# Kernel tuning notes

Measured on AMD Instinct MI355X. Metric: run time of the kernel, lower is better.

The kernel has to match this reference:

```python
import jax, jax.numpy as jnp
import numpy as np

BATCH, E = 4096, 8
DIMS = [512, 1024, 1024, 512]


def setup_inputs() -> dict:
    key = jax.random.key(0)
    ks = jax.random.split(key, 8)
    inp = {
        'weight_blend': jax.random.uniform(ks[0], (BATCH, E), dtype=jnp.float32),
        'x': jax.random.normal(ks[1], (BATCH, DIMS[0]), dtype=jnp.float32),
    }
    for i in range(3):
        inp[f'W{i}'] = jax.random.normal(ks[2 + i], (E, DIMS[i + 1], DIMS[i]), dtype=jnp.float32)
        inp[f'B{i}'] = jnp.zeros((E, DIMS[i + 1]), dtype=jnp.float32)
    return inp


def _blended_layer(weight_blend, x, W, B):
    # Fused form of: weight = sum_e blend[b,e]*W[e]; y = bmm(weight, x) + sum_e blend[b,e]*B[e]
    # Computed as sum_e blend_e * (W_e @ x) without materializing (batch,out,in).
    y = jnp.einsum('eoi,bi->beo', W, x)          # per-expert GEMM, (B,E,out)
    y = jnp.einsum('be,beo->bo', weight_blend, y)  # blend combine
    return y + weight_blend @ B                   # blended bias (B,out)


def reference(weight_blend, x, W0, B0, W1, B1, W2, B2):
    # Dropout with keep_prob=0.0 is identity in eval mode; activations: elu, elu, linear.
    h = jax.nn.elu(_blended_layer(weight_blend, x, W0, B0))
    h = jax.nn.elu(_blended_layer(weight_blend, h, W1, B1))
    out = _blended_layer(weight_blend, h, W2, B2)
    return out
```

## Files before the change

kernel.cpp:

```cpp
#include <hip/hip_runtime.h>
#include <cstdint>
#include <cstddef>

typedef __bf16 bf16x8 __attribute__((ext_vector_type(8)));
typedef float f32x4 __attribute__((ext_vector_type(4)));
typedef unsigned short u16;
typedef unsigned short u16x8 __attribute__((ext_vector_type(8)));

#define BATCH 4096
#define NE 8

__device__ __forceinline__ u16 f2bf(float f) {
  union { float f; uint32_t u; } v; v.f = f;
  uint32_t u = v.u;
  u += 0x7fffu + ((u >> 16) & 1u);
  return (u16)(u >> 16);
}

__device__ __forceinline__ float bf2f(u16 u) {
  union { uint32_t u; float f; } v; v.u = ((uint32_t)u) << 16;
  return v.f;
}

__device__ __forceinline__ void cast8(const float* src, u16* dst) {
  const float4* p = (const float4*)src;
  float4 a = p[0], b = p[1];
  u16x8 o;
  o[0] = f2bf(a.x); o[1] = f2bf(a.y); o[2] = f2bf(a.z); o[3] = f2bf(a.w);
  o[4] = f2bf(b.x); o[5] = f2bf(b.y); o[6] = f2bf(b.z); o[7] = f2bf(b.w);
  *(u16x8*)dst = o;
}

__device__ __forceinline__ void conv_w_chunk(const float* __restrict__ W,
                                             u16* __restrict__ Bt,
                                             int N, int K0, int chunk) {
  int per_row = K0 >> 3;
  int rid = chunk / per_row;
  int i0 = (chunk - rid * per_row) << 3;
  int e = rid / N;
  int o = rid - e * N;
  cast8(W + (size_t)rid * K0 + i0,
        Bt + (size_t)o * ((size_t)NE * K0) + (size_t)e * K0 + i0);
}

__global__ void prep_kernel(const float* __restrict__ x,
                            const float* __restrict__ W0,
                            const float* __restrict__ W1,
                            const float* __restrict__ W2,
                            u16* __restrict__ h0, u16* __restrict__ Bt0,
                            u16* __restrict__ Bt1, u16* __restrict__ Bt2) {
  int t = blockIdx.x * blockDim.x + threadIdx.x;
  const int C0 = BATCH * 512 / 8;
  const int C1 = C0 + NE * 1024 * 512 / 8;
  const int C2 = C1 + NE * 1024 * 1024 / 8;
  if (t < C0) {
    cast8(x + (size_t)t * 8, h0 + (size_t)t * 8);
  } else if (t < C1) {
    conv_w_chunk(W0, Bt0, 1024, 512, t - C0);
  } else if (t < C2) {
    conv_w_chunk(W1, Bt1, 1024, 1024, t - C1);
  } else {
    conv_w_chunk(W2, Bt2, 512, 1024, t - C2);
  }
}

template<int SLICES, bool ELU_ACT, bool OUT_BF16>
__global__ void combineS_kernel(const u16* __restrict__ P,
                                const float* __restrict__ blend,
                                const float* __restrict__ Bias,
                                void* __restrict__ outp, int N) {
  int t = blockIdx.x * blockDim.x + threadIdx.x;
  int per_row = N >> 3;
  int b = t / per_row;
  int i0 = (t - b * per_row) << 3;
  const size_t slice = (size_t)BATCH * N;
  float v[8] = {0, 0, 0, 0, 0, 0, 0, 0};
  #pragma unroll
  for (int s = 0; s < SLICES; ++s) {
    u16x8 pv = *(const u16x8*)(P + (size_t)s * slice + (size_t)b * N + i0);
    #pragma unroll
    for (int j = 0; j < 8; ++j) v[j] += bf2f(pv[j]);
  }
  const float4* blp = (const float4*)(blend + b * NE);
  float4 u0 = blp[0], u1 = blp[1];
  float bl[8] = {u0.x, u0.y, u0.z, u0.w, u1.x, u1.y, u1.z, u1.w};
  #pragma unroll
  for (int e = 0; e < NE; ++e) {
    const float4* bp = (const float4*)(Bias + (size_t)e * N + i0);
    float4 ba = bp[0], bb = bp[1];
    float bv[8] = {ba.x, ba.y, ba.z, ba.w, bb.x, bb.y, bb.z, bb.w};
    #pragma unroll
    for (int j = 0; j < 8; ++j) v[j] += bl[e] * bv[j];
  }
  if (ELU_ACT) {
    #pragma unroll
    for (int j = 0; j < 8; ++j) v[j] = v[j] > 0.f ? v[j] : expm1f(v[j]);
  }
  if (OUT_BF16) {
    u16x8 o;
    #pragma unroll
    for (int j = 0; j < 8; ++j) o[j] = f2bf(v[j]);
    *(u16x8*)((u16*)outp + (size_t)b * N + i0) = o;
  } else {
    float4* op = (float4*)((float*)outp + (size_t)b * N + i0);
    op[0] = (float4){v[0], v[1], v[2], v[3]};
    op[1] = (float4){v[4], v[5], v[6], v[7]};
  }
}

#define GL2LDS(g, l) __builtin_amdgcn_global_load_lds( \
    (__attribute__((address_space(1))) void*)(g),      \
    (__attribute__((address_space(3))) void*)(l), 16, 0, 0)

template<int K0, int EPB>
__global__ __launch_bounds__(256, 2)
void gemm_fold_kernel(const u16* __restrict__ h, const u16* __restrict__ Bt,
                      const float* __restrict__ blend,
                      u16* __restrict__ P, int N) {
  __shared__ __align__(16) u16 Hs[128 * 64];
  __shared__ __align__(16) u16 Bs[128 * 64];
  __shared__ float bls[128 * 9];

  const int tid  = threadIdx.x;
  const int w    = tid >> 6, lane = tid & 63;
  const int wm   = w >> 1,   wn   = w & 1;
  const int lrow = lane & 15, quad = lane >> 4;

  const int row0 = blockIdx.x * 128;
  const int col0 = blockIdx.y * 128;
  const int e0   = blockIdx.z * EPB;
  const int EK   = K0 * NE;

  {
    const float4 bv = ((const float4*)(blend + (size_t)row0 * NE))[tid];
    int row = tid >> 1, c0 = (tid & 1) * 4;
    bls[row * 9 + c0 + 0] = bv.x;
    bls[row * 9 + c0 + 1] = bv.y;
    bls[row * 9 + c0 + 2] = bv.z;
    bls[row * 9 + c0 + 3] = bv.w;
  }

  const int trow = tid >> 3;
  const int tcol = (tid & 7) ^ (trow & 7);
  const u16* gH = h + (size_t)(row0 + trow) * K0 + (tcol << 3);
  const u16* gB = Bt + (size_t)(col0 + trow) * EK + (size_t)e0 * K0 + (tcol << 3);
  u16* lH = &Hs[tid * 8];
  u16* lB = &Bs[tid * 8];

  const int xr = lrow & 7;
  const u16* fH[2][4];
  const u16* fB[2][4];
  #pragma unroll
  for (int kc = 0; kc < 2; ++kc)
    #pragma unroll
    for (int i = 0; i < 4; ++i) {
      fH[kc][i] = &Hs[(wm * 64 + i * 16 + lrow) * 64 + (((kc * 4 + quad) ^ xr) << 3)];
      fB[kc][i] = &Bs[(wn * 64 + i * 16 + lrow) * 64 + (((kc * 4 + quad) ^ xr) << 3)];
    }

  f32x4 acc[4][4];
  #pragma unroll
  for (int i = 0; i < 4; ++i)
    #pragma unroll
    for (int j = 0; j < 4; ++j) acc[i][j] = (f32x4){0.f, 0.f, 0.f, 0.f};

  #pragma unroll 1
  for (int ee = 0; ee < EPB; ++ee) {
    f32x4 acc2[4][4];
    #pragma unroll
    for (int i = 0; i < 4; ++i)
      #pragma unroll
      for (int j = 0; j < 4; ++j) acc2[i][j] = (f32x4){0.f, 0.f, 0.f, 0.f};

    const u16* pH = gH;
    const u16* pB = gB + (size_t)ee * K0;

    for (int it = 0; it < K0 / 64; ++it) {
      #pragma unroll
      for (int i = 0; i < 4; ++i) {
        GL2LDS(pH + (size_t)(32 * i) * K0, lH + 2048 * i);
        GL2LDS(pB + (size_t)(32 * i) * EK, lB + 2048 * i);
      }
      pH += 64; pB += 64;
      __syncthreads();

      #pragma unroll
      for (int kc = 0; kc < 2; ++kc) {
        bf16x8 hf[4], bfr[4];
        #pragma unroll
        for (int i = 0; i < 4; ++i) hf[i] = *(const bf16x8*)fH[kc][i];
        #pragma unroll
        for (int j = 0; j < 4; ++j) bfr[j] = *(const bf16x8*)fB[kc][j];
        #pragma unroll
        for (int i = 0; i < 4; ++i)
          #pragma unroll
          for (int j = 0; j < 4; ++j)
            acc2[i][j] = __builtin_amdgcn_mfma_f32_16x16x32_bf16(hf[i], bfr[j], acc2[i][j], 0, 0, 0);
      }
      __syncthreads();
    }

    #pragma unroll
    for (int mt = 0; mt < 4; ++mt) {
      float bl[4];
      #pragma unroll
      for (int r = 0; r < 4; ++r)
        bl[r] = bls[(wm * 64 + mt * 16 + quad * 4 + r) * 9 + (e0 + ee)];
      #pragma unroll
      for (int nt = 0; nt < 4; ++nt)
        #pragma unroll
        for (int r = 0; r < 4; ++r)
          acc[mt][nt][r] += bl[r] * acc2[mt][nt][r];
    }
  }

  u16* Ps = P + (size_t)blockIdx.z * ((size_t)BATCH * N);
  u16* ls = &Hs[w * 2048];
  #pragma unroll
  for (int half = 0; half < 2; ++half) {
    #pragma unroll
    for (int mh = 0; mh < 2; ++mh) {
      int mt = half * 2 + mh;
      #pragma unroll
      for (int r = 0; r < 4; ++r) {
        int rloc = mh * 16 + quad * 4 + r;
        #pragma unroll
        for (int nt = 0; nt < 4; ++nt) {
          int col = nt * 16 + lrow;
          int c8 = (col >> 3) ^ (rloc & 7);
          ls[rloc * 64 + (c8 << 3) + (col & 7)] = f2bf(acc[mt][nt][r]);
        }
      }
    }
    #pragma unroll
    for (int p = 0; p < 4; ++p) {
      int rloc = p * 8 + (lane >> 3);
      int c8 = (lane & 7) ^ (rloc & 7);
      u16x8 v = *(const u16x8*)&ls[rloc * 64 + (c8 << 3)];
      int row = row0 + wm * 64 + half * 32 + rloc;
      int colg = col0 + wn * 64 + ((lane & 7) << 3);
      *(u16x8*)&Ps[(size_t)row * N + colg] = v;
    }
  }
}

extern "C" void kernel_launch(void* const* d_in, const int* in_sizes, int n_in,
                              void* d_out, int out_size, void* d_ws, size_t ws_size,
                              hipStream_t stream) {
  const float* blend = (const float*)d_in[0];
  const float* x  = (const float*)d_in[1];
  const float* W0 = (const float*)d_in[2];
  const float* B0 = (const float*)d_in[3];
  const float* W1 = (const float*)d_in[4];
  const float* B1 = (const float*)d_in[5];
  const float* W2 = (const float*)d_in[6];
  const float* B2 = (const float*)d_in[7];
  float* out = (float*)d_out;

  char* ws = (char*)d_ws;
  u16* hA  = (u16*)ws;
  u16* h1  = (u16*)(ws + 8388608);
  u16* Bt0 = (u16*)(ws + 16777216);
  u16* Bt1 = (u16*)(ws + 25165824);
  u16* Bt2 = (u16*)(ws + 41943040);
  u16* P   = (u16*)(ws + 50331648);

  prep_kernel<<<9216, 256, 0, stream>>>(x, W0, W1, W2, hA, Bt0, Bt1, Bt2);

  gemm_fold_kernel<512, 4><<<dim3(32, 8, 2), 256, 0, stream>>>(hA, Bt0, blend, P, 1024);
  combineS_kernel<2, true, true><<<2048, 256, 0, stream>>>(P, blend, B0, h1, 1024);

  gemm_fold_kernel<1024, 4><<<dim3(32, 8, 2), 256, 0, stream>>>(h1, Bt1, blend, P, 1024);
  combineS_kernel<2, true, true><<<2048, 256, 0, stream>>>(P, blend, B1, hA, 1024);

  gemm_fold_kernel<1024, 2><<<dim3(32, 4, 4), 256, 0, stream>>>(hA, Bt2, blend, P, 512);
  combineS_kernel<4, false, false><<<1024, 256, 0, stream>>>(P, blend, B2, out, 512);
}
```

Baseline: 287.5 us.

## Pre-swizzle operands into MFMA fragment layout and drop LDS staging in GEMM

Prep and combine kernels now write activations and weights in a 16x32 fragment-tiled layout, so each lane can load its MFMA operand directly from global memory. The GEMM no longer stages tiles through LDS and no longer needs barriers in the K loop. The per-expert blend is folded with a ratio rescaling (acc *= blend_e/blend_{e+1}) so a single accumulator set is kept instead of two. This removes the LDS round trip and the barriers, at the cost of the cache reuse that shared tiles provided. The ratio trick is numerically fragile: blend is clamped at 1e-30, and division by small weights can amplify error.

After: 293.8 us. 1.02x slower.

```diff
diff --git a/kernel.cpp b/kernel.cpp
--- a/kernel.cpp
+++ b/kernel.cpp
@@ -31,40 +31,44 @@
   *(u16x8*)dst = o;
 }
 
-__device__ __forceinline__ void conv_w_chunk(const float* __restrict__ W,
-                                             u16* __restrict__ Bt,
-                                             int N, int K0, int chunk) {
-  int per_row = K0 >> 3;
-  int rid = chunk / per_row;
-  int i0 = (chunk - rid * per_row) << 3;
-  int e = rid / N;
-  int o = rid - e * N;
-  cast8(W + (size_t)rid * K0 + i0,
-        Bt + (size_t)o * ((size_t)NE * K0) + (size_t)e * K0 + i0);
-}
 
 __global__ void prep_kernel(const float* __restrict__ x,
                             const float* __restrict__ W0,
                             const float* __restrict__ W1,
                             const float* __restrict__ W2,
-                            u16* __restrict__ h0, u16* __restrict__ Bt0,
+                            u16* __restrict__ h0f, u16* __restrict__ Bt0,
                             u16* __restrict__ Bt1, u16* __restrict__ Bt2) {
   int t = blockIdx.x * blockDim.x + threadIdx.x;
-  const int C0 = BATCH * 512 / 8;
-  const int C1 = C0 + NE * 1024 * 512 / 8;
-  const int C2 = C1 + NE * 1024 * 1024 / 8;
+  const int C0 = 262144;
+  const int C1 = C0 + 524288;
+  const int C2 = C1 + 1048576;
   if (t < C0) {
-    cast8(x + (size_t)t * 8, h0 + (size_t)t * 8);
+    int lane = t & 63, c = t >> 6;
+    int rowt = c >> 4, kb = c & 15;
+    const float* s = x + ((size_t)(rowt * 16 + (lane & 15)) * 512 + kb * 32 + ((lane >> 4) << 3));
+    cast8(s, h0f + (size_t)c * 512 + (lane << 3));
   } else if (t < C1) {
-    conv_w_chunk(W0, Bt0, 1024, 512, t - C0);
+    int u = t - C0, lane = u & 63, c = u >> 6;
+    int kb = c & 15, c2 = c >> 4;
+    int colt = c2 & 63, e = c2 >> 6;
+    const float* s = W0 + (((size_t)e * 1024 + colt * 16 + (lane & 15)) * 512 + kb * 32 + ((lane >> 4) << 3));
+    cast8(s, Bt0 + (size_t)c * 512 + (lane << 3));
   } else if (t < C2) {
-    conv_w_chunk(W1, Bt1, 1024, 1024, t - C1);
+    int u = t - C1, lane = u & 63, c = u >> 6;
+    int kb = c & 31, c2 = c >> 5;
+    int colt = c2 & 63, e = c2 >> 6;
+    const float* s = W1 + (((size_t)e * 1024 + colt * 16 + (lane & 15)) * 1024 + kb * 32 + ((lane >> 4) << 3));
+    cast8(s, Bt1 + (size_t)c * 512 + (lane << 3));
   } else {
-    conv_w_chunk(W2, Bt2, 512, 1024, t - C2);
-  }
-}
-
-template<int SLICES, bool ELU_ACT, bool OUT_BF16>
+    int u = t - C2, lane = u & 63, c = u >> 6;
+    int kb = c & 31, c2 = c >> 5;
+    int colt = c2 & 31, e = c2 >> 5;
+    const float* s = W2 + (((size_t)e * 512 + colt * 16 + (lane & 15)) * 1024 + kb * 32 + ((lane >> 4) << 3));
+    cast8(s, Bt2 + (size_t)c * 512 + (lane << 3));
+  }
+}
+
+template<int SLICES, bool ELU_ACT, int KN>
 __global__ void combineS_kernel(const u16* __restrict__ P,
                                 const float* __restrict__ blend,
                                 const float* __restrict__ Bias,
@@ -96,11 +100,13 @@
     #pragma unroll
     for (int j = 0; j < 8; ++j) v[j] = v[j] > 0.f ? v[j] : expm1f(v[j]);
   }
-  if (OUT_BF16) {
+  if (KN > 0) {
     u16x8 o;
     #pragma unroll
     for (int j = 0; j < 8; ++j) o[j] = f2bf(v[j]);
-    *(u16x8*)((u16*)outp + (size_t)b * N + i0) = o;
+    int rowt = b >> 4, kb = i0 >> 5;
+    int lane = (b & 15) + (((i0 >> 3) & 3) << 4);
+    *(u16x8*)((u16*)outp + ((size_t)(rowt * (KN >> 5) + kb)) * 512 + (lane << 3)) = o;
   } else {
     float4* op = (float4*)((float*)outp + (size_t)b * N + i0);
     op[0] = (float4){v[0], v[1], v[2], v[3]};
@@ -108,55 +114,38 @@
   }
 }
 
-#define GL2LDS(g, l) __builtin_amdgcn_global_load_lds( \
-    (__attribute__((address_space(1))) void*)(g),      \
-    (__attribute__((address_space(3))) void*)(l), 16, 0, 0)
-
 template<int K0, int EPB>
 __global__ __launch_bounds__(256, 2)
-void gemm_fold_kernel(const u16* __restrict__ h, const u16* __restrict__ Bt,
-                      const float* __restrict__ blend,
-                      u16* __restrict__ P, int N) {
-  __shared__ __align__(16) u16 Hs[128 * 64];
-  __shared__ __align__(16) u16 Bs[128 * 64];
-  __shared__ float bls[128 * 9];
+void gemm_ff_kernel(const u16* __restrict__ Af, const u16* __restrict__ Btf,
+                    const float* __restrict__ blend, u16* __restrict__ P, int N) {
+  constexpr int KB = K0 / 32;
+  __shared__ float rat[128 * EPB];
+  __shared__ __align__(16) u16 ls[4 * 2048];
 
   const int tid  = threadIdx.x;
   const int w    = tid >> 6, lane = tid & 63;
   const int wm   = w >> 1,   wn   = w & 1;
   const int lrow = lane & 15, quad = lane >> 4;
-
   const int row0 = blockIdx.x * 128;
   const int col0 = blockIdx.y * 128;
   const int e0   = blockIdx.z * EPB;
-  const int EK   = K0 * NE;
-
-  {
-    const float4 bv = ((const float4*)(blend + (size_t)row0 * NE))[tid];
-    int row = tid >> 1, c0 = (tid & 1) * 4;
-    bls[row * 9 + c0 + 0] = bv.x;
-    bls[row * 9 + c0 + 1] = bv.y;
-    bls[row * 9 + c0 + 2] = bv.z;
-    bls[row * 9 + c0 + 3] = bv.w;
-  }
-
-  const int trow = tid >> 3;
-  const int tcol = (tid & 7) ^ (trow & 7);
-  const u16* gH = h + (size_t)(row0 + trow) * K0 + (tcol << 3);
-  const u16* gB = Bt + (size_t)(col0 + trow) * EK + (size_t)e0 * K0 + (tcol << 3);
-  u16* lH = &Hs[tid * 8];
-  u16* lB = &Bs[tid * 8];
-
-  const int xr = lrow & 7;
-  const u16* fH[2][4];
-  const u16* fB[2][4];
-  #pragma unroll
-  for (int kc = 0; kc < 2; ++kc)
-    #pragma unroll
-    for (int i = 0; i < 4; ++i) {
-      fH[kc][i] = &Hs[(wm * 64 + i * 16 + lrow) * 64 + (((kc * 4 + quad) ^ xr) << 3)];
-      fB[kc][i] = &Bs[(wn * 64 + i * 16 + lrow) * 64 + (((kc * 4 + quad) ^ xr) << 3)];
-    }
+  const int NT   = N >> 4;
+
+  for (int t = tid; t < 128 * EPB; t += 256) {
+    int row = t / EPB, j = t % EPB;
+    float sa = fmaxf(blend[(size_t)(row0 + row) * NE + e0 + j], 1e-30f);
+    float sb = (j < EPB - 1) ? fmaxf(blend[(size_t)(row0 + row) * NE + e0 + j + 1], 1e-30f) : 1.0f;
+    rat[t] = sa / sb;
+  }
+  __syncthreads();
+
+  const u16* aA[4];
+  const u16* aB[4];
+  #pragma unroll
+  for (int i = 0; i < 4; ++i) {
+    aA[i] = Af  + ((size_t)(blockIdx.x * 8 + wm * 4 + i) * KB) * 512 + (lane << 3);
+    aB[i] = Btf + ((size_t)((e0 * NT) + blockIdx.y * 8 + wn * 4 + i) * KB) * 512 + (lane << 3);
+  }
 
   f32x4 acc[4][4];
   #pragma unroll
@@ -166,56 +155,45 @@
 
   #pragma unroll 1
   for (int ee = 0; ee < EPB; ++ee) {
-    f32x4 acc2[4][4];
-    #pragma unroll
-    for (int i = 0; i < 4; ++i)
-      #pragma unroll
-      for (int j = 0; j < 4; ++j) acc2[i][j] = (f32x4){0.f, 0.f, 0.f, 0.f};
-
-    const u16* pH = gH;
-    const u16* pB = gB + (size_t)ee * K0;
-
-    for (int it = 0; it < K0 / 64; ++it) {
-      #pragma unroll
-      for (int i = 0; i < 4; ++i) {
-        GL2LDS(pH + (size_t)(32 * i) * K0, lH + 2048 * i);
-        GL2LDS(pB + (size_t)(32 * i) * EK, lB + 2048 * i);
-      }
-      pH += 64; pB += 64;
-      __syncthreads();
-
-      #pragma unroll
-      for (int kc = 0; kc < 2; ++kc) {
-        bf16x8 hf[4], bfr[4];
-        #pragma unroll
-        for (int i = 0; i < 4; ++i) hf[i] = *(const bf16x8*)fH[kc][i];
-        #pragma unroll
-        for (int j = 0; j < 4; ++j) bfr[j] = *(const bf16x8*)fB[kc][j];
+    #pragma unroll 1
+    for (int kq = 0; kq < KB / 4; ++kq) {
+      #pragma unroll
+      for (int u = 0; u < 4; ++u) {
+        bf16x8 fa[4], fb[4];
+        #pragma unroll
+        for (int i = 0; i < 4; ++i) fa[i] = *(const bf16x8*)(aA[i] + u * 512);
+        #pragma unroll
+        for (int j = 0; j < 4; ++j) fb[j] = *(const bf16x8*)(aB[j] + u * 512);
         #pragma unroll
         for (int i = 0; i < 4; ++i)
           #pragma unroll
           for (int j = 0; j < 4; ++j)
-            acc2[i][j] = __builtin_amdgcn_mfma_f32_16x16x32_bf16(hf[i], bfr[j], acc2[i][j], 0, 0, 0);
+            acc[i][j] = __builtin_amdgcn_mfma_f32_16x16x32_bf16(fa[i], fb[j], acc[i][j], 0, 0, 0);
       }
-      __syncthreads();
-    }
-
+      #pragma unroll
+      for (int i = 0; i < 4; ++i) { aA[i] += 2048; aB[i] += 2048; }
+    }
     #pragma unroll
     for (int mt = 0; mt < 4; ++mt) {
-      float bl[4];
+      float rr[4];
       #pragma unroll
       for (int r = 0; r < 4; ++r)
-        bl[r] = bls[(wm * 64 + mt * 16 + quad * 4 + r) * 9 + (e0 + ee)];
+        rr[r] = rat[(wm * 64 + mt * 16 + quad * 4 + r) * EPB + ee];
       #pragma unroll
       for (int nt = 0; nt < 4; ++nt)
         #pragma unroll
         for (int r = 0; r < 4; ++r)
-          acc[mt][nt][r] += bl[r] * acc2[mt][nt][r];
+          acc[mt][nt][r] *= rr[r];
+    }
+    #pragma unroll
+    for (int i = 0; i < 4; ++i) {
+      aA[i] -= (size_t)KB * 512;
+      aB[i] += (size_t)(NT - 1) * KB * 512;
     }
   }
 
   u16* Ps = P + (size_t)blockIdx.z * ((size_t)BATCH * N);
-  u16* ls = &Hs[w * 2048];
+  u16* lw = &ls[w * 2048];
   #pragma unroll
   for (int half = 0; half < 2; ++half) {
     #pragma unroll
@@ -228,7 +206,7 @@
         for (int nt = 0; nt < 4; ++nt) {
           int col = nt * 16 + lrow;
           int c8 = (col >> 3) ^ (rloc & 7);
-          ls[rloc * 64 + (c8 << 3) + (col & 7)] = f2bf(acc[mt][nt][r]);
+          lw[rloc * 64 + (c8 << 3) + (col & 7)] = f2bf(acc[mt][nt][r]);
         }
       }
     }
@@ -236,10 +214,10 @@
     for (int p = 0; p < 4; ++p) {
       int rloc = p * 8 + (lane >> 3);
       int c8 = (lane & 7) ^ (rloc & 7);
-      u16x8 v = *(const u16x8*)&ls[rloc * 64 + (c8 << 3)];
+      u16x8 vv = *(const u16x8*)&lw[rloc * 64 + (c8 << 3)];
       int row = row0 + wm * 64 + half * 32 + rloc;
       int colg = col0 + wn * 64 + ((lane & 7) << 3);
-      *(u16x8*)&Ps[(size_t)row * N + colg] = v;
+      *(u16x8*)&Ps[(size_t)row * N + colg] = vv;
     }
   }
 }
@@ -267,12 +245,12 @@
 
   prep_kernel<<<9216, 256, 0, stream>>>(x, W0, W1, W2, hA, Bt0, Bt1, Bt2);
 
-  gemm_fold_kernel<512, 4><<<dim3(32, 8, 2), 256, 0, stream>>>(hA, Bt0, blend, P, 1024);
-  combineS_kernel<2, true, true><<<2048, 256, 0, stream>>>(P, blend, B0, h1, 1024);
-
-  gemm_fold_kernel<1024, 4><<<dim3(32, 8, 2), 256, 0, stream>>>(h1, Bt1, blend, P, 1024);
-  combineS_kernel<2, true, true><<<2048, 256, 0, stream>>>(P, blend, B1, hA, 1024);
-
-  gemm_fold_kernel<1024, 2><<<dim3(32, 4, 4), 256, 0, stream>>>(hA, Bt2, blend, P, 512);
-  combineS_kernel<4, false, false><<<1024, 256, 0, stream>>>(P, blend, B2, out, 512);
-}
+  gemm_ff_kernel<512, 4><<<dim3(32, 8, 2), 256, 0, stream>>>(hA, Bt0, blend, P, 1024);
+  combineS_kernel<2, true, 1024><<<2048, 256, 0, stream>>>(P, blend, B0, h1, 1024);
+
+  gemm_ff_kernel<1024, 4><<<dim3(32, 8, 2), 256, 0, stream>>>(h1, Bt1, blend, P, 1024);
+  combineS_kernel<2, true, 1024><<<2048, 256, 0, stream>>>(P, blend, B1, hA, 1024);
+
+  gemm_ff_kernel<1024, 2><<<dim3(32, 4, 4), 256, 0, stream>>>(hA, Bt2, blend, P, 512);
+  combineS_kernel<4, false, 0><<<1024, 256, 0, stream>>>(P, blend, B2, out, 512);
+}
```
